# Kernel tuning notes

Measured on AMD Instinct MI355X. Metric: run time of the kernel, lower is better.

The kernel has to match this reference:

```python
import jax, jax.numpy as jnp
import numpy as np

LRELU_GAIN = np.sqrt(2.0).astype(np.float32)  # apply_activation gain for leaky_relu


def setup_inputs() -> dict:
    key = jax.random.key(0)
    ks = jax.random.split(key, 8)
    N, H, W, C_in = 8, 256, 256, 128
    num_ws, w_dim, fmaps, kernel = 16, 512, 128, 3
    return {
        "x": jax.random.normal(ks[0], (N, H, W, C_in), dtype=jnp.float32),
        "dlatents": jax.random.normal(ks[1], (N, num_ws, w_dim), dtype=jnp.float32),
        "noise": jax.random.normal(ks[2], (N, H, W, 1), dtype=jnp.float32),
        "affine_w": jax.random.normal(ks[3], (w_dim, C_in), dtype=jnp.float32),
        "affine_b": jnp.ones((C_in,), dtype=jnp.float32),  # bias_init=1
        "conv_w": jax.random.normal(ks[4], (kernel, kernel, C_in, fmaps), dtype=jnp.float32),
        "conv_b": jax.random.normal(ks[5], (fmaps,), dtype=jnp.float32),
        "noise_strength": jax.random.uniform(ks[6], (1,), dtype=jnp.float32),
        "layer_idx": 5,
    }


def reference(x, dlatents, noise, affine_w, affine_b, conv_w, conv_b, noise_strength, layer_idx):
    # --- affine (equalized-lr Linear, lr_multiplier=1): s = z @ (W/sqrt(fan_in)) + b ---
    w_dim = affine_w.shape[0]
    z = dlatents[:, layer_idx]                                   # [N, w_dim]
    s = z @ (affine_w * np.float32(1.0 / np.sqrt(w_dim))) + affine_b   # [N, C_in]

    # --- equalized-lr conv weight: w * 1/sqrt(k*k*C_in) ---
    k, _, cin, cout = conv_w.shape
    w = conv_w * np.float32(1.0 / np.sqrt(k * k * cin))          # [k,k,Cin,Cout]

    # --- demodulation coefficient d[n,o] = rsqrt(sum_{k,k,i} (w*s)^2 + eps) ---
    d = jax.lax.rsqrt(jnp.einsum('hwio,ni->no', jnp.square(w), jnp.square(s)) + 1e-8)  # [N, Cout]

    # --- non-fused modconv: modulate input, shared conv, demodulate output ---
    xm = x * s[:, None, None, :]                                 # [N,H,W,Cin]
    y = jax.lax.conv_general_dilated(
        xm, w, window_strides=(1, 1), padding='SAME',
        dimension_numbers=('NHWC', 'HWIO', 'NHWC'))              # [N,H,W,Cout]
    y = y * d[:, None, None, :]

    # --- noise injection, bias, activation (leaky_relu 0.2 with sqrt(2) gain) ---
    y = y + noise_strength[0] * noise
    y = y + conv_b
    return jax.nn.leaky_relu(y, negative_slope=0.2) * LRELU_GAIN
```

## Files before the change

kernel.cpp:

```cpp
#include <hip/hip_runtime.h>

typedef unsigned short u16;
typedef unsigned int   u32;
typedef __bf16 v8bf __attribute__((ext_vector_type(8)));
typedef float  v4f  __attribute__((ext_vector_type(4)));

#define INV_SQRT_W   0.044194173824159216f
#define INV_SQRT_KKC 0.029462782549439483f
#define LRELU_GAIN   1.4142135623730951f

__device__ __forceinline__ u16 f2bf(float f) {
    u32 u = __float_as_uint(f);
    u = (u + 0x7fffu + ((u >> 16) & 1u)) >> 16;
    return (u16)u;
}

__device__ __forceinline__ void glds16(const u16* g, u16* l) {
    __builtin_amdgcn_global_load_lds(
        (const __attribute__((address_space(1))) void*)g,
        (__attribute__((address_space(3))) void*)l, 16, 0, 0);
}

__global__ void k_s(const float* __restrict__ dlat,
                    const float* __restrict__ aw,
                    const float* __restrict__ ab,
                    const int*   __restrict__ lidx,
                    float* __restrict__ s_out)
{
    const int n   = blockIdx.x;
    const int tid = threadIdx.x;
    const int i   = tid & 127, kh = tid >> 7;
    const int li  = lidx[0];
    const float* z = dlat + (n * 16 + li) * 512 + kh * 256;
    const float* a = aw + kh * 256 * 128 + i;
    float a0 = 0.f, a1 = 0.f, a2 = 0.f, a3 = 0.f;
    for (int k = 0; k < 256; k += 4) {
        a0 += z[k + 0] * a[(k + 0) * 128];
        a1 += z[k + 1] * a[(k + 1) * 128];
        a2 += z[k + 2] * a[(k + 2) * 128];
        a3 += z[k + 3] * a[(k + 3) * 128];
    }
    __shared__ float part[256];
    part[tid] = a0 + a1 + a2 + a3;
    __syncthreads();
    if (tid < 128)
        s_out[n * 128 + i] = (part[i] + part[i + 128]) * INV_SQRT_W + ab[i];
}

__global__ void k_w2(const float* __restrict__ cw, float* __restrict__ W2)
{
    const int idx = blockIdx.x * 256 + threadIdx.x;
    float acc = 0.f;
    #pragma unroll
    for (int t = 0; t < 9; ++t) {
        float w = cw[t * 16384 + idx];
        acc += w * w;
    }
    W2[idx] = acc * (INV_SQRT_KKC * INV_SQRT_KKC);
}

__global__ void k_d(const float* __restrict__ W2,
                    const float* __restrict__ s_buf,
                    float* __restrict__ d_out)
{
    const int n = blockIdx.x;
    const int o = threadIdx.x;
    __shared__ float s2[128];
    float sv = s_buf[n * 128 + o];
    s2[o] = sv * sv;
    __syncthreads();
    float acc = 1e-8f;
    #pragma unroll 4
    for (int i = 0; i < 128; ++i)
        acc += W2[i * 128 + o] * s2[i];
    d_out[n * 128 + o] = 1.0f / sqrtf(acc);
}

__global__ void k_wmod(const float* __restrict__ cw,
                       const float* __restrict__ s_buf,
                       const float* __restrict__ d_buf,
                       u16* __restrict__ wmod)
{
    const int b   = blockIdx.x;
    const int n   = b / 36;
    const int s   = b - n * 36;
    const int q4  = s / 9;
    const int r   = s - q4 * 9;
    const int tw  = r / 3, th = r - tw * 3;
    const int tap = th * 3 + tw;
    const int cibase = q4 * 32;
    const int tid = threadIdx.x;
    __shared__ float ssh[32], dsh[128];
    if (tid < 32)  ssh[tid] = s_buf[n * 128 + cibase + tid] * INV_SQRT_KKC;
    if (tid < 128) dsh[tid] = d_buf[n * 128 + tid];
    __syncthreads();
    u16* wt = wmod + ((size_t)b << 12);
    #pragma unroll
    for (int rep = 0; rep < 2; ++rep) {
        int t2   = rep * 256 + tid;
        int g    = t2 >> 7;
        int cout = t2 & 127;
        float dv = dsh[cout];
        u32 pk[4];
        #pragma unroll
        for (int jj = 0; jj < 4; ++jj) {
            int cl = g * 8 + jj * 2;
            float v0 = cw[((tap * 128 + cibase + cl) << 7) + cout]     * ssh[cl]     * dv;
            float v1 = cw[((tap * 128 + cibase + cl + 1) << 7) + cout] * ssh[cl + 1] * dv;
            pk[jj] = (u32)f2bf(v0) | ((u32)f2bf(v1) << 16);
        }
        *(uint4*)&wt[(g << 10) + (cout << 3)] = *(uint4*)pk;
    }
}

template<int T>
__device__ __forceinline__ void conv_step(const u16* __restrict__ wn,
                                          u16* __restrict__ bsh,
                                          const u16* a_base,
                                          const u16* b_lane,
                                          v8bf af[6], v4f acc[4][4],
                                          int wid, int lane)
{
    constexpr int q4 = T / 9, r = T % 9, tw = r / 3, th = r % 3;
    constexpr int slot = T % 3;
    constexpr int hq = q4 & 1;
    if constexpr (T == 0 || T == 18)
        asm volatile("s_waitcnt vmcnt(2) lgkmcnt(0)" ::: "memory");
    else if constexpr (T == 35)
        asm volatile("s_waitcnt vmcnt(0)" ::: "memory");
    else
        asm volatile("s_waitcnt vmcnt(2)" ::: "memory");
    __builtin_amdgcn_s_barrier();
    asm volatile("" ::: "memory");

    v8bf bf[4];
    #pragma unroll
    for (int ni = 0; ni < 4; ++ni)
        bf[ni] = *(const v8bf*)(b_lane + slot * 4096 + (ni << 7));
    if constexpr (th == 0) {
        #pragma unroll
        for (int j = 0; j < 6; ++j)
            af[j] = *(const v8bf*)(a_base + hq * 5792 + (j * 18 + tw) * 8);
    }
    if constexpr (T + 2 < 36) {
        constexpr int ns = (T + 2) % 3;
        #pragma unroll
        for (int t = 0; t < 2; ++t) {
            int chunk = wid + (t << 2);
            glds16(wn + (T + 2) * 4096 + (chunk << 9) + (lane << 3),
                   &bsh[ns * 4096 + (chunk << 9) + (lane << 3)]);
        }
    }
    #pragma unroll
    for (int mi = 0; mi < 4; ++mi)
        #pragma unroll
        for (int ni = 0; ni < 4; ++ni)
            acc[mi][ni] = __builtin_amdgcn_mfma_f32_16x16x32_bf16(
                af[mi + th], bf[ni], acc[mi][ni], 0, 0, 0);
}

__global__ __launch_bounds__(256, 3) void k_conv(
    const float* __restrict__ x,
    const float* __restrict__ noise,
    const float* __restrict__ conv_b,
    const float* __restrict__ nstr,
    const u16*   __restrict__ wmod,
    float* __restrict__ out)
{
    __shared__ __align__(16) u16 xs[11584];
    __shared__ __align__(16) u16 bsh[12288];

    const int bid0 = blockIdx.x;
    const int bid  = ((bid0 & 7) << 9) + (bid0 >> 3);
    const int n   = bid >> 9;
    const int hb  = (bid >> 4) & 31;
    const int wb  = bid & 15;
    const int h0  = hb << 3, w0 = wb << 4;

    const int tid  = threadIdx.x;
    const int lane = tid & 63;
    const int wid  = tid >> 6;
    const int wm   = wid >> 1;
    const int wq   = wid & 1;
    const int lr   = lane & 15;
    const int kg   = lane >> 4;

    const float* xbase = x + ((size_t)n << 16) * 128;

    #define STAGE_X(ph)                                                              \
    for (int t = tid; t < 1440; t += 256) {                                          \
        int q = t >> 3, g = t & 7;                                                   \
        int rr_ = q / 18, cc = q - rr_ * 18;                                         \
        int gh = h0 + rr_ - 1, gw = w0 + cc - 1;                                     \
        float v0=0.f,v1=0.f,v2=0.f,v3=0.f,v4=0.f,v5=0.f,v6=0.f,v7=0.f;               \
        if ((unsigned)gh < 256u && (unsigned)gw < 256u) {                            \
            const float* src = xbase + (size_t)((gh << 8) + gw) * 128                \
                               + (ph) * 64 + (g << 3);                               \
            float4 fa = *(const float4*)(src);                                       \
            float4 fb = *(const float4*)(src + 4);                                   \
            v0=fa.x; v1=fa.y; v2=fa.z; v3=fa.w; v4=fb.x; v5=fb.y; v6=fb.z; v7=fb.w;  \
        }                                                                            \
        v8bf pk;                                                                     \
        pk[0]=(__bf16)v0; pk[1]=(__bf16)v1; pk[2]=(__bf16)v2; pk[3]=(__bf16)v3;      \
        pk[4]=(__bf16)v4; pk[5]=(__bf16)v5; pk[6]=(__bf16)v6; pk[7]=(__bf16)v7;      \
        *(v8bf*)&xs[g * 1448 + q * 8] = pk;                                          \
    }

    STAGE_X(0)

    const u16* wn = wmod + ((size_t)n * 36) * 4096;
    #pragma unroll
    for (int s0 = 0; s0 < 2; ++s0)
        #pragma unroll
        for (int t = 0; t < 2; ++t) {
            int chunk = wid + (t << 2);
            glds16(wn + s0 * 4096 + (chunk << 9) + (lane << 3),
                   &bsh[s0 * 4096 + (chunk << 9) + (lane << 3)]);
        }

    v4f acc[4][4];
    #pragma unroll
    for (int a = 0; a < 4; ++a)
        #pragma unroll
        for (int b2 = 0; b2 < 4; ++b2) {
            v4f zz = {0.f, 0.f, 0.f, 0.f};
            acc[a][b2] = zz;
        }

    const u16* const a_base = &xs[kg * 1448 + (wm * 72 + lr) * 8];
    const u16* const b_lane = &bsh[kg * 1024 + (wq * 64 + lr) * 8];

    v8bf af[6];
    conv_step< 0>(wn, bsh, a_base, b_lane, af, acc, wid, lane);
    conv_step< 1>(wn, bsh, a_base, b_lane, af, acc, wid, lane);
    conv_step< 2>(wn, bsh, a_base, b_lane, af, acc, wid, lane);
    conv_step< 3>(wn, bsh, a_base, b_lane, af, acc, wid, lane);
    conv_step< 4>(wn, bsh, a_base, b_lane, af, acc, wid, lane);
    conv_step< 5>(wn, bsh, a_base, b_lane, af, acc, wid, lane);
    conv_step< 6>(wn, bsh, a_base, b_lane, af, acc, wid, lane);
    conv_step< 7>(wn, bsh, a_base, b_lane, af, acc, wid, lane);
    conv_step< 8>(wn, bsh, a_base, b_lane, af, acc, wid, lane);
    conv_step< 9>(wn, bsh, a_base, b_lane, af, acc, wid, lane);
    conv_step<10>(wn, bsh, a_base, b_lane, af, acc, wid, lane);
    conv_step<11>(wn, bsh, a_base, b_lane, af, acc, wid, lane);
    conv_step<12>(wn, bsh, a_base, b_lane, af, acc, wid, lane);
    conv_step<13>(wn, bsh, a_base, b_lane, af, acc, wid, lane);
    conv_step<14>(wn, bsh, a_base, b_lane, af, acc, wid, lane);
    conv_step<15>(wn, bsh, a_base, b_lane, af, acc, wid, lane);
    conv_step<16>(wn, bsh, a_base, b_lane, af, acc, wid, lane);
    conv_step<17>(wn, bsh, a_base, b_lane, af, acc, wid, lane);

    STAGE_X(1)

    conv_step<18>(wn, bsh, a_base, b_lane, af, acc, wid, lane);
    conv_step<19>(wn, bsh, a_base, b_lane, af, acc, wid, lane);
    conv_step<20>(wn, bsh, a_base, b_lane, af, acc, wid, lane);
    conv_step<21>(wn, bsh, a_base, b_lane, af, acc, wid, lane);
    conv_step<22>(wn, bsh, a_base, b_lane, af, acc, wid, lane);
    conv_step<23>(wn, bsh, a_base, b_lane, af, acc, wid, lane);
    conv_step<24>(wn, bsh, a_base, b_lane, af, acc, wid, lane);
    conv_step<25>(wn, bsh, a_base, b_lane, af, acc, wid, lane);
    conv_step<26>(wn, bsh, a_base, b_lane, af, acc, wid, lane);
    conv_step<27>(wn, bsh, a_base, b_lane, af, acc, wid, lane);
    conv_step<28>(wn, bsh, a_base, b_lane, af, acc, wid, lane);
    conv_step<29>(wn, bsh, a_base, b_lane, af, acc, wid, lane);
    conv_step<30>(wn, bsh, a_base, b_lane, af, acc, wid, lane);
    conv_step<31>(wn, bsh, a_base, b_lane, af, acc, wid, lane);
    conv_step<32>(wn, bsh, a_base, b_lane, af, acc, wid, lane);
    conv_step<33>(wn, bsh, a_base, b_lane, af, acc, wid, lane);
    conv_step<34>(wn, bsh, a_base, b_lane, af, acc, wid, lane);
    conv_step<35>(wn, bsh, a_base, b_lane, af, acc, wid, lane);

    const float ns = nstr[0];
    float cb4[4];
    #pragma unroll
    for (int ni = 0; ni < 4; ++ni)
        cb4[ni] = conv_b[wq * 64 + ni * 16 + lr];
    #pragma unroll
    for (int mi = 0; mi < 4; ++mi) {
        const int h = h0 + wm * 4 + mi;
        #pragma unroll
        for (int j = 0; j < 4; ++j) {
            const int w  = w0 + kg * 4 + j;
            const float nz = noise[((n << 8) + h) * 256 + w] * ns;
            float* orow = out + (size_t)((((n << 8) + h) << 8) + w) * 128;
            #pragma unroll
            for (int ni = 0; ni < 4; ++ni) {
                const int cout = wq * 64 + ni * 16 + lr;
                float v = acc[mi][ni][j] + nz + cb4[ni];
                v = (v < 0.f ? 0.2f * v : v) * LRELU_GAIN;
                orow[cout] = v;
            }
        }
    }
}

extern "C" void kernel_launch(void* const* d_in, const int* in_sizes, int n_in,
                              void* d_out, int out_size, void* d_ws, size_t ws_size,
                              hipStream_t stream) {
    const float* x     = (const float*)d_in[0];
    const float* dlat  = (const float*)d_in[1];
    const float* noise = (const float*)d_in[2];
    const float* aw    = (const float*)d_in[3];
    const float* ab    = (const float*)d_in[4];
    const float* cw    = (const float*)d_in[5];
    const float* cb    = (const float*)d_in[6];
    const float* nstr  = (const float*)d_in[7];
    const int*   lidx  = (const int*)d_in[8];
    float* out = (float*)d_out;

    float* s_buf = (float*)d_ws;
    float* d_buf = (float*)((char*)d_ws + 4096);
    float* W2    = (float*)((char*)d_ws + 8192);
    u16*   wmod  = (u16*)((char*)d_ws + 8192);

    k_w2  <<<64,  256, 0, stream>>>(cw, W2);
    k_s   <<<8,   256, 0, stream>>>(dlat, aw, ab, lidx, s_buf);
    k_d   <<<8,   128, 0, stream>>>(W2, s_buf, d_buf);
    k_wmod<<<288, 256, 0, stream>>>(cw, s_buf, d_buf, wmod);
    k_conv<<<4096,256, 0, stream>>>(x, noise, cb, nstr, wmod, out);
}
```

Baseline: 217.6 us.

## Enlarge conv tile to 16x16 pixels with 512-thread blocks; split affine GEMV

The conv kernel now covers a 16x16 spatial tile per block with 8 waves instead of 8x16 with 4 waves. This cuts the halo overhead in the x staging and halves the per-output loads of the modulated weights. Each wave now issues one weight chunk per step, so the vmcnt waits drop from 2 to 1. Launch bounds become (512,4), which tightens the VGPR budget, and LDS use grows to about 66KB, so occupancy may fall and registers may spill. The affine GEMV is also split into a 32-block partial-sum kernel plus a reduction kernel to spread it across more blocks.

```diff
diff --git a/kernel.cpp b/kernel.cpp
--- a/kernel.cpp
+++ b/kernel.cpp
@@ -21,30 +21,39 @@
         (__attribute__((address_space(3))) void*)l, 16, 0, 0);
 }
 
-__global__ void k_s(const float* __restrict__ dlat,
-                    const float* __restrict__ aw,
-                    const float* __restrict__ ab,
-                    const int*   __restrict__ lidx,
-                    float* __restrict__ s_out)
-{
-    const int n   = blockIdx.x;
+__global__ void k_s1(const float* __restrict__ dlat,
+                     const float* __restrict__ aw,
+                     const int*   __restrict__ lidx,
+                     float* __restrict__ part)
+{
+    const int b   = blockIdx.x;
+    const int n   = b >> 2, kh = b & 3;
     const int tid = threadIdx.x;
-    const int i   = tid & 127, kh = tid >> 7;
+    const int i   = tid & 127, half = tid >> 7;
     const int li  = lidx[0];
-    const float* z = dlat + (n * 16 + li) * 512 + kh * 256;
-    const float* a = aw + kh * 256 * 128 + i;
-    float a0 = 0.f, a1 = 0.f, a2 = 0.f, a3 = 0.f;
-    for (int k = 0; k < 256; k += 4) {
-        a0 += z[k + 0] * a[(k + 0) * 128];
+    const float* z = dlat + (n * 16 + li) * 512 + kh * 128 + half * 64;
+    const float* a = aw + (kh * 128 + half * 64) * 128 + i;
+    float a0 = 0.f, a1 = 0.f;
+    #pragma unroll 8
+    for (int k = 0; k < 64; k += 2) {
+        a0 += z[k]     * a[k * 128];
         a1 += z[k + 1] * a[(k + 1) * 128];
-        a2 += z[k + 2] * a[(k + 2) * 128];
-        a3 += z[k + 3] * a[(k + 3) * 128];
-    }
-    __shared__ float part[256];
-    part[tid] = a0 + a1 + a2 + a3;
+    }
+    __shared__ float red[256];
+    red[tid] = a0 + a1;
     __syncthreads();
     if (tid < 128)
-        s_out[n * 128 + i] = (part[i] + part[i + 128]) * INV_SQRT_W + ab[i];
+        part[b * 128 + i] = red[i] + red[i + 128];
+}
+
+__global__ void k_s2(const float* __restrict__ part,
+                     const float* __restrict__ ab,
+                     float* __restrict__ s_out)
+{
+    const int n = blockIdx.x, i = threadIdx.x;
+    float s = part[(n * 4 + 0) * 128 + i] + part[(n * 4 + 1) * 128 + i]
+            + part[(n * 4 + 2) * 128 + i] + part[(n * 4 + 3) * 128 + i];
+    s_out[n * 128 + i] = s * INV_SQRT_W + ab[i];
 }
 
 __global__ void k_w2(const float* __restrict__ cw, float* __restrict__ W2)
@@ -125,11 +134,11 @@
     constexpr int slot = T % 3;
     constexpr int hq = q4 & 1;
     if constexpr (T == 0 || T == 18)
-        asm volatile("s_waitcnt vmcnt(2) lgkmcnt(0)" ::: "memory");
+        asm volatile("s_waitcnt vmcnt(1) lgkmcnt(0)" ::: "memory");
     else if constexpr (T == 35)
         asm volatile("s_waitcnt vmcnt(0)" ::: "memory");
     else
-        asm volatile("s_waitcnt vmcnt(2)" ::: "memory");
+        asm volatile("s_waitcnt vmcnt(1)" ::: "memory");
     __builtin_amdgcn_s_barrier();
     asm volatile("" ::: "memory");
 
@@ -140,16 +149,12 @@
     if constexpr (th == 0) {
         #pragma unroll
         for (int j = 0; j < 6; ++j)
-            af[j] = *(const v8bf*)(a_base + hq * 5792 + (j * 18 + tw) * 8);
+            af[j] = *(const v8bf*)(a_base + hq * 10400 + (j * 18 + tw) * 8);
     }
     if constexpr (T + 2 < 36) {
         constexpr int ns = (T + 2) % 3;
-        #pragma unroll
-        for (int t = 0; t < 2; ++t) {
-            int chunk = wid + (t << 2);
-            glds16(wn + (T + 2) * 4096 + (chunk << 9) + (lane << 3),
-                   &bsh[ns * 4096 + (chunk << 9) + (lane << 3)]);
-        }
+        glds16(wn + (T + 2) * 4096 + (wid << 9) + (lane << 3),
+               &bsh[ns * 4096 + (wid << 9) + (lane << 3)]);
     }
     #pragma unroll
     for (int mi = 0; mi < 4; ++mi)
@@ -159,7 +164,7 @@
                 af[mi + th], bf[ni], acc[mi][ni], 0, 0, 0);
 }
 
-__global__ __launch_bounds__(256, 3) void k_conv(
+__global__ __launch_bounds__(512, 4) void k_conv(
     const float* __restrict__ x,
     const float* __restrict__ noise,
     const float* __restrict__ conv_b,
@@ -167,28 +172,28 @@
     const u16*   __restrict__ wmod,
     float* __restrict__ out)
 {
-    __shared__ __align__(16) u16 xs[11584];
+    __shared__ __align__(16) u16 xs[20800];
     __shared__ __align__(16) u16 bsh[12288];
 
     const int bid0 = blockIdx.x;
-    const int bid  = ((bid0 & 7) << 9) + (bid0 >> 3);
-    const int n   = bid >> 9;
-    const int hb  = (bid >> 4) & 31;
+    const int bid  = ((bid0 & 7) << 8) + (bid0 >> 3);
+    const int n   = bid >> 8;
+    const int hb  = (bid >> 4) & 15;
     const int wb  = bid & 15;
-    const int h0  = hb << 3, w0 = wb << 4;
+    const int h0  = hb << 4, w0 = wb << 4;
 
     const int tid  = threadIdx.x;
     const int lane = tid & 63;
     const int wid  = tid >> 6;
     const int wm   = wid >> 1;
-    const int wq   = wid & 1;
+    const int wn_  = wid & 1;
     const int lr   = lane & 15;
     const int kg   = lane >> 4;
 
     const float* xbase = x + ((size_t)n << 16) * 128;
 
     #define STAGE_X(ph)                                                              \
-    for (int t = tid; t < 1440; t += 256) {                                          \
+    for (int t = tid; t < 2592; t += 512) {                                          \
         int q = t >> 3, g = t & 7;                                                   \
         int rr_ = q / 18, cc = q - rr_ * 18;                                         \
         int gh = h0 + rr_ - 1, gw = w0 + cc - 1;                                     \
@@ -203,7 +208,7 @@
         v8bf pk;                                                                     \
         pk[0]=(__bf16)v0; pk[1]=(__bf16)v1; pk[2]=(__bf16)v2; pk[3]=(__bf16)v3;      \
         pk[4]=(__bf16)v4; pk[5]=(__bf16)v5; pk[6]=(__bf16)v6; pk[7]=(__bf16)v7;      \
-        *(v8bf*)&xs[g * 1448 + q * 8] = pk;                                          \
+        *(v8bf*)&xs[g * 2600 + q * 8] = pk;                                          \
     }
 
     STAGE_X(0)
@@ -211,12 +216,8 @@
     const u16* wn = wmod + ((size_t)n * 36) * 4096;
     #pragma unroll
     for (int s0 = 0; s0 < 2; ++s0)
-        #pragma unroll
-        for (int t = 0; t < 2; ++t) {
-            int chunk = wid + (t << 2);
-            glds16(wn + s0 * 4096 + (chunk << 9) + (lane << 3),
-                   &bsh[s0 * 4096 + (chunk << 9) + (lane << 3)]);
-        }
+        glds16(wn + s0 * 4096 + (wid << 9) + (lane << 3),
+               &bsh[s0 * 4096 + (wid << 9) + (lane << 3)]);
 
     v4f acc[4][4];
     #pragma unroll
@@ -227,8 +228,8 @@
             acc[a][b2] = zz;
         }
 
-    const u16* const a_base = &xs[kg * 1448 + (wm * 72 + lr) * 8];
-    const u16* const b_lane = &bsh[kg * 1024 + (wq * 64 + lr) * 8];
+    const u16* const a_base = &xs[kg * 2600 + (wm * 72 + lr) * 8];
+    const u16* const b_lane = &bsh[kg * 1024 + (wn_ * 64 + lr) * 8];
 
     v8bf af[6];
     conv_step< 0>(wn, bsh, a_base, b_lane, af, acc, wid, lane);
@@ -275,7 +276,7 @@
     float cb4[4];
     #pragma unroll
     for (int ni = 0; ni < 4; ++ni)
-        cb4[ni] = conv_b[wq * 64 + ni * 16 + lr];
+        cb4[ni] = conv_b[wn_ * 64 + ni * 16 + lr];
     #pragma unroll
     for (int mi = 0; mi < 4; ++mi) {
         const int h = h0 + wm * 4 + mi;
@@ -286,7 +287,7 @@
             float* orow = out + (size_t)((((n << 8) + h) << 8) + w) * 128;
             #pragma unroll
             for (int ni = 0; ni < 4; ++ni) {
-                const int cout = wq * 64 + ni * 16 + lr;
+                const int cout = wn_ * 64 + ni * 16 + lr;
                 float v = acc[mi][ni][j] + nz + cb4[ni];
                 v = (v < 0.f ? 0.2f * v : v) * LRELU_GAIN;
                 orow[cout] = v;
@@ -313,10 +314,12 @@
     float* d_buf = (float*)((char*)d_ws + 4096);
     float* W2    = (float*)((char*)d_ws + 8192);
     u16*   wmod  = (u16*)((char*)d_ws + 8192);
+    float* part  = (float*)((char*)d_ws + 8192 + 2359296);
 
     k_w2  <<<64,  256, 0, stream>>>(cw, W2);
-    k_s   <<<8,   256, 0, stream>>>(dlat, aw, ab, lidx, s_buf);
+    k_s1  <<<32,  256, 0, stream>>>(dlat, aw, lidx, part);
+    k_s2  <<<8,   128, 0, stream>>>(part, ab, s_buf);
     k_d   <<<8,   128, 0, stream>>>(W2, s_buf, d_buf);
     k_wmod<<<288, 256, 0, stream>>>(cw, s_buf, d_buf, wmod);
-    k_conv<<<4096,256, 0, stream>>>(x, noise, cb, nstr, wmod, out);
-}
+    k_conv<<<2048,512, 0, stream>>>(x, noise, cb, nstr, wmod, out);
+}
```

New measurement: 195.0 us (median of 2 runs). 1.12x faster.
